# Optimization experiments

Measured on AMD Instinct MI355X. Metric: run time of the kernel, lower is better.

Reference implementation:

```python
import jax, jax.numpy as jnp
import numpy as np

K_BITS = 4
V_BITS = 4
GROUP_SIZE = 64
EPS = 1e-8


def _quant_dequant_per_token(x, bits):
    # TurboQuantProd: symmetric per-token (per head_dim vector) absmax quantization.
    qmax = 2.0 ** (bits - 1) - 1.0
    scale = jnp.maximum(jnp.max(jnp.abs(x), axis=-1, keepdims=True) / qmax, EPS)
    return jnp.clip(jnp.round(x / scale), -qmax, qmax) * scale


def _quant_dequant_grouped(x, bits, group_size):
    # TurboQuantValue: symmetric grouped absmax quantization along head_dim.
    shp = x.shape
    xg = x.reshape(shp[:-1] + (shp[-1] // group_size, group_size))
    qmax = 2.0 ** (bits - 1) - 1.0
    scale = jnp.maximum(jnp.max(jnp.abs(xg), axis=-1, keepdims=True) / qmax, EPS)
    dq = jnp.clip(jnp.round(xg / scale), -qmax, qmax) * scale
    return dq.reshape(shp)


def setup_inputs() -> dict:
    key = jax.random.key(0)
    kq, kk, kv = jax.random.split(key, 3)
    B, H, S, D = 2, 16, 2048, 128
    query = jax.random.normal(kq, (B, H, S, D), dtype=jnp.float32)
    k = jax.random.normal(kk, (B, H, S, D), dtype=jnp.float32)
    v = jax.random.normal(kv, (B, H, S, D), dtype=jnp.float32)
    causal_mask = jnp.tril(jnp.ones((S, S), dtype=bool))[None, None]  # [1,1,S,S]
    return {"query": query, "key": k, "value": v, "causal_mask": causal_mask}


def reference(query, key, value, causal_mask):
    # Non-protected path: quantize K per-token, V grouped, then fused dequant + SDPA.
    head_dim = query.shape[-1]
    scale = 1.0 / np.sqrt(head_dim).astype(np.float32)
    dq_key = _quant_dequant_per_token(key, K_BITS)
    dq_value = _quant_dequant_grouped(value, V_BITS, GROUP_SIZE)
    scores = jnp.einsum('bhqd,bhkd->bhqk', query, dq_key) * scale
    scores = jnp.where(causal_mask, scores, -jnp.inf)
    weights = jax.nn.softmax(scores, axis=-1)
    output = jnp.einsum('bhqk,bhkd->bhqd', weights, dq_value)
    return (output, weights)
```

## Files before the change

kernel.cpp:

```cpp
#include <hip/hip_runtime.h>

#define SQ 2048
#define DD 128
#define BHN 32
#define SC2 0.12751741934f

typedef __attribute__((ext_vector_type(8))) short bf16x8;
typedef __attribute__((ext_vector_type(4))) float f32x4;

__device__ __forceinline__ unsigned short f2bf(float x){
  unsigned int u = __float_as_uint(x);
  unsigned int r = (u + 0x7FFFu + ((u >> 16) & 1u)) >> 16;
  return (unsigned short)r;
}
__device__ __forceinline__ unsigned pack2bf(float a, float b){
  return (unsigned)f2bf(a) | ((unsigned)f2bf(b) << 16);
}

__device__ __forceinline__ void gl_lds16(const void* g, void* l){
  __builtin_amdgcn_global_load_lds(
      (const __attribute__((address_space(1))) unsigned int*)g,
      (__attribute__((address_space(3))) unsigned int*)l, 16, 0, 0);
}

__global__ __launch_bounds__(256) void qd_kernel(const float* __restrict__ K,
                                                 const float* __restrict__ V,
                                                 char* __restrict__ dqK,
                                                 char* __restrict__ dqVt){
  __shared__ float Vlds[128*65];
  const int t = threadIdx.x;
  const int bh = blockIdx.x >> 5;
  const int stile = blockIdx.x & 31;
  const int tt = t >> 2;
  const int q4 = t & 3;
  const int s = stile*64 + tt;
  const long ebase = ((long)(bh*SQ + s))*DD + 32*q4;

  float vals[32];
  {
    const float4* kp = (const float4*)(K + ebase);
    float am = 0.f;
    #pragma unroll
    for (int j=0;j<8;j++){
      float4 v4 = kp[j];
      vals[4*j+0]=v4.x; vals[4*j+1]=v4.y; vals[4*j+2]=v4.z; vals[4*j+3]=v4.w;
      am = fmaxf(am, fmaxf(fmaxf(fabsf(v4.x),fabsf(v4.y)),fmaxf(fabsf(v4.z),fabsf(v4.w))));
    }
    am = fmaxf(am, __shfl_xor(am,1));
    am = fmaxf(am, __shfl_xor(am,2));
    const float sc = fmaxf(am/7.0f, 1e-8f);
    #pragma unroll
    for (int j=0;j<32;j++){
      float qv = rintf(vals[j]/sc);
      qv = fminf(7.f, fmaxf(-7.f, qv));
      vals[j] = qv*sc;
    }
    const long rowb = ((long)(bh*SQ + s))*256;
    const int swz = (s & 7) << 4;
    #pragma unroll
    for (int c=0;c<4;c++){
      uint4 w;
      w.x = pack2bf(vals[8*c+0], vals[8*c+1]);
      w.y = pack2bf(vals[8*c+2], vals[8*c+3]);
      w.z = pack2bf(vals[8*c+4], vals[8*c+5]);
      w.w = pack2bf(vals[8*c+6], vals[8*c+7]);
      *(uint4*)(dqK + rowb + ((64*q4 + 16*c) ^ swz)) = w;
    }
  }
  {
    const float4* vp = (const float4*)(V + ebase);
    float am = 0.f;
    #pragma unroll
    for (int j=0;j<8;j++){
      float4 v4 = vp[j];
      vals[4*j+0]=v4.x; vals[4*j+1]=v4.y; vals[4*j+2]=v4.z; vals[4*j+3]=v4.w;
      am = fmaxf(am, fmaxf(fmaxf(fabsf(v4.x),fabsf(v4.y)),fmaxf(fabsf(v4.z),fabsf(v4.w))));
    }
    am = fmaxf(am, __shfl_xor(am,1));
    const float sc = fmaxf(am/7.0f, 1e-8f);
    #pragma unroll
    for (int j=0;j<32;j++){
      float qv = rintf(vals[j]/sc);
      qv = fminf(7.f, fmaxf(-7.f, qv));
      Vlds[(32*q4 + j)*65 + tt] = qv*sc;
    }
  }
  __syncthreads();
  #pragma unroll
  for (int m=0;m<4;m++){
    const int chunk = m*256 + t;
    const int d = chunk >> 3;
    const int c = chunk & 7;
    uint4 w;
    const float* f = &Vlds[d*65 + 8*c];
    w.x = pack2bf(f[0], f[1]);
    w.y = pack2bf(f[2], f[3]);
    w.z = pack2bf(f[4], f[5]);
    w.w = pack2bf(f[6], f[7]);
    const long ob = ((long)(bh*DD + d))*4096 + (long)stile*128 + ((16*c) ^ ((d&7)<<4));
    *(uint4*)(dqVt + ob) = w;
  }
}

__global__ __launch_bounds__(256,2) void attn1_kernel(const float* __restrict__ Q,
    const char* __restrict__ dqK, const char* __restrict__ dqVt,
    float* __restrict__ Out, float* __restrict__ SinvG){
  __shared__ __attribute__((aligned(16))) char Kt[2][16384];
  __shared__ __attribute__((aligned(16))) char Vt[2][16384];
  __shared__ __attribute__((aligned(16))) char Et[4][4096];

  const int bid = blockIdx.x;
  const int xcd = bid & 7;
  const int loc = bid >> 3;
  const int bh  = xcd*4 + (loc & 3);
  const int p   = loc >> 2;
  const int t = threadIdx.x;
  const int lane = t & 63;
  const int w = t >> 6;
  const int s = w >> 1;
  const int ws = w & 1;
  const int l15 = lane & 15, l4 = lane >> 4;
  const int swz = (l15 & 7) << 4;

  const int qt   = s ? p : (31 - p);
  const int q0   = qt * 64;
  const int nktA = 32 - p;
  const int myNkt = qt + 1;
  const int rbase = q0 + 32*ws;

  bf16x8 qa[2][4];
  #pragma unroll
  for (int g=0; g<2; ++g){
    const float* qb = Q + ((long)(bh*SQ) + rbase + 16*g + l15)*DD + 8*l4;
    #pragma unroll
    for (int kk=0;kk<4;kk++){
      float4 a = *(const float4*)(qb + 32*kk);
      float4 b = *(const float4*)(qb + 32*kk + 4);
      bf16x8 r;
      r[0]=(short)f2bf(a.x); r[1]=(short)f2bf(a.y); r[2]=(short)f2bf(a.z); r[3]=(short)f2bf(a.w);
      r[4]=(short)f2bf(b.x); r[5]=(short)f2bf(b.y); r[6]=(short)f2bf(b.z); r[7]=(short)f2bf(b.w);
      qa[g][kk]=r;
    }
  }

  const char* Kb = dqK + (long)bh*SQ*256;
  const char* Vb = dqVt + (long)bh*DD*4096;

  const f32x4 z4 = {0.f,0.f,0.f,0.f};
  f32x4 oacc[2][8] = {{z4,z4,z4,z4,z4,z4,z4,z4},{z4,z4,z4,z4,z4,z4,z4,z4}};
  float ssum[2] = {0.f, 0.f};
  char* eb = &Et[w][0];

  auto stage = [&](int buf, int kt){
    const char* ks = Kb + (long)kt*16384;
    #pragma unroll
    for (int i=0;i<4;i++)
      gl_lds16(ks + i*4096 + t*16, &Kt[buf][i*4096 + t*16]);
    const char* vs = Vb + (long)kt*128;
    #pragma unroll
    for (int i=0;i<4;i++)
      gl_lds16(vs + (long)(i*32 + (t>>3))*4096 + (t&7)*16, &Vt[buf][i*4096 + t*16]);
  };

  stage(0, 0);
  __syncthreads();
  int cur = 0;
  for (int kt=0; kt<nktA; ++kt){
    if (kt+1 < nktA) stage(cur^1, kt+1);

    if (kt < myNkt){
      f32x4 sacc[2][4] = {{z4,z4,z4,z4},{z4,z4,z4,z4}};
      {
        const char* kbase = &Kt[cur][0] + l15*256;
        __builtin_amdgcn_s_setprio(1);
        #pragma unroll
        for (int cf=0;cf<4;cf++){
          #pragma unroll
          for (int kk=0;kk<4;kk++){
            bf16x8 kb = *(const bf16x8*)(kbase + cf*4096 + ((64*kk+16*l4) ^ swz));
            sacc[0][cf] = __builtin_amdgcn_mfma_f32_16x16x32_bf16(kb, qa[0][kk], sacc[0][cf], 0,0,0);
            sacc[1][cf] = __builtin_amdgcn_mfma_f32_16x16x32_bf16(kb, qa[1][kk], sacc[1][cf], 0,0,0);
          }
        }
        __builtin_amdgcn_s_setprio(0);
      }

      const int k0 = kt*64;
      if (kt < qt){
        #pragma unroll
        for (int g=0; g<2; ++g){
          const int lr = 16*g + l15;
          #pragma unroll
          for (int cf=0;cf<4;cf++){
            float e0 = exp2f(sacc[g][cf][0]*SC2);
            float e1 = exp2f(sacc[g][cf][1]*SC2);
            float e2 = exp2f(sacc[g][cf][2]*SC2);
            float e3 = exp2f(sacc[g][cf][3]*SC2);
            ssum[g] += (e0+e1) + (e2+e3);
            uint2 wp; wp.x = pack2bf(e0,e1); wp.y = pack2bf(e2,e3);
            *(uint2*)(eb + lr*128 + ((32*cf + 8*l4) ^ swz)) = wp;
          }
        }
      } else {
        #pragma unroll
        for (int g=0; g<2; ++g){
          const int lr = 16*g + l15;
          const int qrow = rbase + lr;
          #pragma unroll
          for (int cf=0;cf<4;cf++){
            const int tok0 = k0 + 16*cf + 4*l4;
            float e0 = (tok0+0 <= qrow) ? exp2f(sacc[g][cf][0]*SC2) : 0.f;
            float e1 = (tok0+1 <= qrow) ? exp2f(sacc[g][cf][1]*SC2) : 0.f;
            float e2 = (tok0+2 <= qrow) ? exp2f(sacc[g][cf][2]*SC2) : 0.f;
            float e3 = (tok0+3 <= qrow) ? exp2f(sacc[g][cf][3]*SC2) : 0.f;
            ssum[g] += (e0+e1) + (e2+e3);
            uint2 wp; wp.x = pack2bf(e0,e1); wp.y = pack2bf(e2,e3);
            *(uint2*)(eb + lr*128 + ((32*cf + 8*l4) ^ swz)) = wp;
          }
        }
      }

      {
        const char* vbase = &Vt[cur][0] + l15*128;
        __builtin_amdgcn_s_setprio(1);
        #pragma unroll
        for (int kc=0;kc<2;kc++){
          const int eo = (64*kc + 16*l4) ^ swz;
          bf16x8 ea0 = *(const bf16x8*)(eb + l15*128 + eo);
          bf16x8 ea1 = *(const bf16x8*)(eb + (16+l15)*128 + eo);
          #pragma unroll
          for (int df=0;df<8;df++){
            bf16x8 vv = *(const bf16x8*)(vbase + df*2048 + eo);
            oacc[0][df] = __builtin_amdgcn_mfma_f32_16x16x32_bf16(ea0, vv, oacc[0][df], 0,0,0);
            oacc[1][df] = __builtin_amdgcn_mfma_f32_16x16x32_bf16(ea1, vv, oacc[1][df], 0,0,0);
          }
        }
        __builtin_amdgcn_s_setprio(0);
      }
    }
    __syncthreads();
    cur ^= 1;
  }

  #pragma unroll
  for (int g=0; g<2; ++g){
    float sm = ssum[g];
    sm += __shfl_xor(sm, 16);
    sm += __shfl_xor(sm, 32);
    const float sinv = 1.0f / sm;
    if (l4 == 0) SinvG[(long)bh*SQ + rbase + 16*g + l15] = sinv;
    float invr[4];
    #pragma unroll
    for (int i=0;i<4;i++) invr[i] = __shfl(sinv, 4*l4+i);
    float* ob = Out + ((long)(bh*SQ) + rbase + 16*g)*DD;
    #pragma unroll
    for (int df=0;df<8;df++){
      #pragma unroll
      for (int i=0;i<4;i++)
        ob[(4*l4+i)*DD + 16*df + l15] = oacc[g][df][i]*invr[i];
    }
  }
}

__global__ __launch_bounds__(256) void attn2_kernel(const float* __restrict__ Q,
    const char* __restrict__ dqK, const float* __restrict__ SinvG,
    float* __restrict__ Wout){
  __shared__ __attribute__((aligned(16))) char Kt[2][16384];

  const int bid = blockIdx.x;
  const int qt  = bid >> 5;
  const int r   = bid & 31;
  const int bh  = 4*(r & 7) + (r >> 3);
  const int q0  = qt * 64;
  const int t = threadIdx.x;
  const int lane = t & 63;
  const int w = t >> 6;
  const int l15 = lane & 15, l4 = lane >> 4;
  const int swz = (l15 & 7) << 4;
  const int qrow = q0 + 16*w + l15;

  bf16x8 qa[4];
  {
    const float* qb = Q + ((long)(bh*SQ) + qrow)*DD + 8*l4;
    #pragma unroll
    for (int kk=0;kk<4;kk++){
      float4 a = *(const float4*)(qb + 32*kk);
      float4 b = *(const float4*)(qb + 32*kk + 4);
      bf16x8 r2;
      r2[0]=(short)f2bf(a.x); r2[1]=(short)f2bf(a.y); r2[2]=(short)f2bf(a.z); r2[3]=(short)f2bf(a.w);
      r2[4]=(short)f2bf(b.x); r2[5]=(short)f2bf(b.y); r2[6]=(short)f2bf(b.z); r2[7]=(short)f2bf(b.w);
      qa[kk]=r2;
    }
  }
  const float si = SinvG[(long)bh*SQ + qrow];
  const char* Kb = dqK + (long)bh*SQ*256;
  const int nkt = qt + 1;
  float* Wbase = Wout + (long)bh*SQ*SQ;
  float* wrow  = Wbase + (long)qrow*SQ;

  auto stage = [&](int buf, int kt){
    const char* ks = Kb + (long)kt*16384;
    #pragma unroll
    for (int i=0;i<4;i++)
      gl_lds16(ks + i*4096 + t*16, &Kt[buf][i*4096 + t*16]);
  };

  stage(0,0);
  __syncthreads();
  int cur = 0;
  const f32x4 z4 = {0.f,0.f,0.f,0.f};
  for (int kt=0; kt<nkt; ++kt){
    if (kt+1 < nkt) stage(cur^1, kt+1);
    const int k0 = kt*64;

    f32x4 sacc[4] = {z4,z4,z4,z4};
    {
      const char* kbase = &Kt[cur][0] + l15*256;
      __builtin_amdgcn_s_setprio(1);
      #pragma unroll
      for (int cf=0;cf<4;cf++){
        #pragma unroll
        for (int kk=0;kk<4;kk++){
          bf16x8 kb = *(const bf16x8*)(kbase + cf*4096 + ((64*kk+16*l4) ^ swz));
          sacc[cf] = __builtin_amdgcn_mfma_f32_16x16x32_bf16(kb, qa[kk], sacc[cf], 0,0,0);
        }
      }
      __builtin_amdgcn_s_setprio(0);
    }

    if (kt < qt){
      #pragma unroll
      for (int cf=0;cf<4;cf++){
        const int tok0 = k0 + 16*cf + 4*l4;
        float4 wv;
        wv.x = exp2f(sacc[cf][0]*SC2)*si;
        wv.y = exp2f(sacc[cf][1]*SC2)*si;
        wv.z = exp2f(sacc[cf][2]*SC2)*si;
        wv.w = exp2f(sacc[cf][3]*SC2)*si;
        *(float4*)(wrow + tok0) = wv;
      }
    } else {
      #pragma unroll
      for (int cf=0;cf<4;cf++){
        const int tok0 = k0 + 16*cf + 4*l4;
        float4 wv;
        wv.x = (tok0+0 <= qrow) ? exp2f(sacc[cf][0]*SC2)*si : 0.f;
        wv.y = (tok0+1 <= qrow) ? exp2f(sacc[cf][1]*SC2)*si : 0.f;
        wv.z = (tok0+2 <= qrow) ? exp2f(sacc[cf][2]*SC2)*si : 0.f;
        wv.w = (tok0+3 <= qrow) ? exp2f(sacc[cf][3]*SC2)*si : 0.f;
        *(float4*)(wrow + tok0) = wv;
      }
    }
    __syncthreads();
    cur ^= 1;
  }

  const int z0 = nkt*64;
  if (z0 < SQ){
    float* wr = Wbase + (long)(q0 + 16*w)*SQ;
    const float4 zz = {0.f,0.f,0.f,0.f};
    for (int rr=0;rr<16;rr++){
      float* row = wr + (long)rr*SQ;
      for (int c = z0 + 4*lane; c < SQ; c += 256)
        *(float4*)(row + c) = zz;
    }
  }
}

extern "C" void kernel_launch(void* const* d_in, const int* in_sizes, int n_in,
                              void* d_out, int out_size, void* d_ws, size_t ws_size,
                              hipStream_t stream) {
  const float* Q = (const float*)d_in[0];
  const float* K = (const float*)d_in[1];
  const float* V = (const float*)d_in[2];
  float* Out = (float*)d_out;
  float* Wout = (float*)d_out + (size_t)BHN*SQ*DD;
  char* dqK  = (char*)d_ws;
  char* dqVt = (char*)d_ws + (size_t)BHN*SQ*DD*2;
  float* SinvG = (float*)((char*)d_ws + (size_t)BHN*SQ*DD*4);

  qd_kernel<<<BHN*32, 256, 0, stream>>>(K, V, dqK, dqVt);
  attn1_kernel<<<512, 256, 0, stream>>>(Q, dqK, dqVt, Out, SinvG);
  attn2_kernel<<<1024, 256, 0, stream>>>(Q, dqK, SinvG, Wout);
}
```

Before: 272.5 us.

## Fuse weights-output pass into attention kernel, recomputing QK^T after row sums

Merges the second kernel, which recomputed scores and wrote normalized softmax weights, into the first attention kernel as a second pass over K tiles after the row sums are known. This drops one kernel launch, the SinvG round trip through global memory, and the separate Q load and bf16 conversion. In exchange each fused block now does the weight-writing pass serially after the output pass, inheriting the first kernel's 512-block grid and its paired-tile load balancing instead of the 1024-block grid. The large weight-matrix store traffic now competes within fewer blocks.

```diff
diff --git a/kernel.cpp b/kernel.cpp
--- a/kernel.cpp
+++ b/kernel.cpp
@@ -102,9 +102,9 @@
   }
 }
 
-__global__ __launch_bounds__(256,2) void attn1_kernel(const float* __restrict__ Q,
+__global__ __launch_bounds__(256,2) void attn_fused(const float* __restrict__ Q,
     const char* __restrict__ dqK, const char* __restrict__ dqVt,
-    float* __restrict__ Out, float* __restrict__ SinvG){
+    float* __restrict__ Out, float* __restrict__ Wout){
   __shared__ __attribute__((aligned(16))) char Kt[2][16384];
   __shared__ __attribute__((aligned(16))) char Vt[2][16384];
   __shared__ __attribute__((aligned(16))) char Et[4][4096];
@@ -151,7 +151,7 @@
   float ssum[2] = {0.f, 0.f};
   char* eb = &Et[w][0];
 
-  auto stage = [&](int buf, int kt){
+  auto stageKV = [&](int buf, int kt){
     const char* ks = Kb + (long)kt*16384;
     #pragma unroll
     for (int i=0;i<4;i++)
@@ -161,12 +161,18 @@
     for (int i=0;i<4;i++)
       gl_lds16(vs + (long)(i*32 + (t>>3))*4096 + (t&7)*16, &Vt[buf][i*4096 + t*16]);
   };
-
-  stage(0, 0);
+  auto stageK = [&](int buf, int kt){
+    const char* ks = Kb + (long)kt*16384;
+    #pragma unroll
+    for (int i=0;i<4;i++)
+      gl_lds16(ks + i*4096 + t*16, &Kt[buf][i*4096 + t*16]);
+  };
+
+  stageKV(0, 0);
   __syncthreads();
   int cur = 0;
   for (int kt=0; kt<nktA; ++kt){
-    if (kt+1 < nktA) stage(cur^1, kt+1);
+    if (kt+1 < nktA) stageKV(cur^1, kt+1);
 
     if (kt < myNkt){
       f32x4 sacc[2][4] = {{z4,z4,z4,z4},{z4,z4,z4,z4}};
@@ -242,16 +248,16 @@
     cur ^= 1;
   }
 
+  float si[2];
   #pragma unroll
   for (int g=0; g<2; ++g){
     float sm = ssum[g];
     sm += __shfl_xor(sm, 16);
     sm += __shfl_xor(sm, 32);
-    const float sinv = 1.0f / sm;
-    if (l4 == 0) SinvG[(long)bh*SQ + rbase + 16*g + l15] = sinv;
+    si[g] = 1.0f / sm;
     float invr[4];
     #pragma unroll
-    for (int i=0;i<4;i++) invr[i] = __shfl(sinv, 4*l4+i);
+    for (int i=0;i<4;i++) invr[i] = __shfl(si[g], 4*l4+i);
     float* ob = Out + ((long)(bh*SQ) + rbase + 16*g)*DD;
     #pragma unroll
     for (int df=0;df<8;df++){
@@ -260,107 +266,74 @@
         ob[(4*l4+i)*DD + 16*df + l15] = oacc[g][df][i]*invr[i];
     }
   }
-}
-
-__global__ __launch_bounds__(256) void attn2_kernel(const float* __restrict__ Q,
-    const char* __restrict__ dqK, const float* __restrict__ SinvG,
-    float* __restrict__ Wout){
-  __shared__ __attribute__((aligned(16))) char Kt[2][16384];
-
-  const int bid = blockIdx.x;
-  const int qt  = bid >> 5;
-  const int r   = bid & 31;
-  const int bh  = 4*(r & 7) + (r >> 3);
-  const int q0  = qt * 64;
-  const int t = threadIdx.x;
-  const int lane = t & 63;
-  const int w = t >> 6;
-  const int l15 = lane & 15, l4 = lane >> 4;
-  const int swz = (l15 & 7) << 4;
-  const int qrow = q0 + 16*w + l15;
-
-  bf16x8 qa[4];
-  {
-    const float* qb = Q + ((long)(bh*SQ) + qrow)*DD + 8*l4;
-    #pragma unroll
-    for (int kk=0;kk<4;kk++){
-      float4 a = *(const float4*)(qb + 32*kk);
-      float4 b = *(const float4*)(qb + 32*kk + 4);
-      bf16x8 r2;
-      r2[0]=(short)f2bf(a.x); r2[1]=(short)f2bf(a.y); r2[2]=(short)f2bf(a.z); r2[3]=(short)f2bf(a.w);
-      r2[4]=(short)f2bf(b.x); r2[5]=(short)f2bf(b.y); r2[6]=(short)f2bf(b.z); r2[7]=(short)f2bf(b.w);
-      qa[kk]=r2;
-    }
-  }
-  const float si = SinvG[(long)bh*SQ + qrow];
-  const char* Kb = dqK + (long)bh*SQ*256;
-  const int nkt = qt + 1;
+
   float* Wbase = Wout + (long)bh*SQ*SQ;
-  float* wrow  = Wbase + (long)qrow*SQ;
-
-  auto stage = [&](int buf, int kt){
-    const char* ks = Kb + (long)kt*16384;
-    #pragma unroll
-    for (int i=0;i<4;i++)
-      gl_lds16(ks + i*4096 + t*16, &Kt[buf][i*4096 + t*16]);
-  };
-
-  stage(0,0);
   __syncthreads();
-  int cur = 0;
-  const f32x4 z4 = {0.f,0.f,0.f,0.f};
-  for (int kt=0; kt<nkt; ++kt){
-    if (kt+1 < nkt) stage(cur^1, kt+1);
-    const int k0 = kt*64;
-
-    f32x4 sacc[4] = {z4,z4,z4,z4};
-    {
-      const char* kbase = &Kt[cur][0] + l15*256;
-      __builtin_amdgcn_s_setprio(1);
-      #pragma unroll
-      for (int cf=0;cf<4;cf++){
-        #pragma unroll
-        for (int kk=0;kk<4;kk++){
-          bf16x8 kb = *(const bf16x8*)(kbase + cf*4096 + ((64*kk+16*l4) ^ swz));
-          sacc[cf] = __builtin_amdgcn_mfma_f32_16x16x32_bf16(kb, qa[kk], sacc[cf], 0,0,0);
-        }
-      }
-      __builtin_amdgcn_s_setprio(0);
-    }
-
-    if (kt < qt){
-      #pragma unroll
-      for (int cf=0;cf<4;cf++){
-        const int tok0 = k0 + 16*cf + 4*l4;
-        float4 wv;
-        wv.x = exp2f(sacc[cf][0]*SC2)*si;
-        wv.y = exp2f(sacc[cf][1]*SC2)*si;
-        wv.z = exp2f(sacc[cf][2]*SC2)*si;
-        wv.w = exp2f(sacc[cf][3]*SC2)*si;
-        *(float4*)(wrow + tok0) = wv;
-      }
-    } else {
-      #pragma unroll
-      for (int cf=0;cf<4;cf++){
-        const int tok0 = k0 + 16*cf + 4*l4;
-        float4 wv;
-        wv.x = (tok0+0 <= qrow) ? exp2f(sacc[cf][0]*SC2)*si : 0.f;
-        wv.y = (tok0+1 <= qrow) ? exp2f(sacc[cf][1]*SC2)*si : 0.f;
-        wv.z = (tok0+2 <= qrow) ? exp2f(sacc[cf][2]*SC2)*si : 0.f;
-        wv.w = (tok0+3 <= qrow) ? exp2f(sacc[cf][3]*SC2)*si : 0.f;
-        *(float4*)(wrow + tok0) = wv;
+  stageK(0, 0);
+  __syncthreads();
+  cur = 0;
+  for (int kt=0; kt<nktA; ++kt){
+    if (kt+1 < nktA) stageK(cur^1, kt+1);
+
+    if (kt < myNkt){
+      f32x4 sacc[2][4] = {{z4,z4,z4,z4},{z4,z4,z4,z4}};
+      {
+        const char* kbase = &Kt[cur][0] + l15*256;
+        __builtin_amdgcn_s_setprio(1);
+        #pragma unroll
+        for (int cf=0;cf<4;cf++){
+          #pragma unroll
+          for (int kk=0;kk<4;kk++){
+            bf16x8 kb = *(const bf16x8*)(kbase + cf*4096 + ((64*kk+16*l4) ^ swz));
+            sacc[0][cf] = __builtin_amdgcn_mfma_f32_16x16x32_bf16(kb, qa[0][kk], sacc[0][cf], 0,0,0);
+            sacc[1][cf] = __builtin_amdgcn_mfma_f32_16x16x32_bf16(kb, qa[1][kk], sacc[1][cf], 0,0,0);
+          }
+        }
+        __builtin_amdgcn_s_setprio(0);
+      }
+      const int k0 = kt*64;
+      if (kt < qt){
+        #pragma unroll
+        for (int g=0; g<2; ++g){
+          float* wrow = Wbase + (long)(rbase + 16*g + l15)*SQ;
+          #pragma unroll
+          for (int cf=0;cf<4;cf++){
+            const int tok0 = k0 + 16*cf + 4*l4;
+            float4 wv;
+            wv.x = exp2f(sacc[g][cf][0]*SC2)*si[g];
+            wv.y = exp2f(sacc[g][cf][1]*SC2)*si[g];
+            wv.z = exp2f(sacc[g][cf][2]*SC2)*si[g];
+            wv.w = exp2f(sacc[g][cf][3]*SC2)*si[g];
+            *(float4*)(wrow + tok0) = wv;
+          }
+        }
+      } else {
+        #pragma unroll
+        for (int g=0; g<2; ++g){
+          const int qrow = rbase + 16*g + l15;
+          float* wrow = Wbase + (long)qrow*SQ;
+          #pragma unroll
+          for (int cf=0;cf<4;cf++){
+            const int tok0 = k0 + 16*cf + 4*l4;
+            float4 wv;
+            wv.x = (tok0+0 <= qrow) ? exp2f(sacc[g][cf][0]*SC2)*si[g] : 0.f;
+            wv.y = (tok0+1 <= qrow) ? exp2f(sacc[g][cf][1]*SC2)*si[g] : 0.f;
+            wv.z = (tok0+2 <= qrow) ? exp2f(sacc[g][cf][2]*SC2)*si[g] : 0.f;
+            wv.w = (tok0+3 <= qrow) ? exp2f(sacc[g][cf][3]*SC2)*si[g] : 0.f;
+            *(float4*)(wrow + tok0) = wv;
+          }
+        }
       }
     }
     __syncthreads();
     cur ^= 1;
   }
 
-  const int z0 = nkt*64;
+  const int z0 = myNkt*64;
   if (z0 < SQ){
-    float* wr = Wbase + (long)(q0 + 16*w)*SQ;
     const float4 zz = {0.f,0.f,0.f,0.f};
-    for (int rr=0;rr<16;rr++){
-      float* row = wr + (long)rr*SQ;
+    for (int rr=0;rr<32;rr++){
+      float* row = Wbase + (long)(rbase + rr)*SQ;
       for (int c = z0 + 4*lane; c < SQ; c += 256)
         *(float4*)(row + c) = zz;
     }
@@ -377,9 +350,7 @@
   float* Wout = (float*)d_out + (size_t)BHN*SQ*DD;
   char* dqK  = (char*)d_ws;
   char* dqVt = (char*)d_ws + (size_t)BHN*SQ*DD*2;
-  float* SinvG = (float*)((char*)d_ws + (size_t)BHN*SQ*DD*4);
 
   qd_kernel<<<BHN*32, 256, 0, stream>>>(K, V, dqK, dqVt);
-  attn1_kernel<<<512, 256, 0, stream>>>(Q, dqK, dqVt, Out, SinvG);
-  attn2_kernel<<<1024, 256, 0, stream>>>(Q, dqK, SinvG, Wout);
-}
+  attn_fused<<<512, 256, 0, stream>>>(Q, dqK, dqVt, Out, Wout);
+}
```

Result: faster. 242.3 us (-11.1%).
